# Optimization experiments

Hardware: AMD Instinct MI355X
Metric: run time of the kernel (lower is better)

The kernel has to match this reference:

```python
import jax, jax.numpy as jnp
import numpy as np


def setup_inputs() -> dict:
    key = jax.random.key(0)
    k1, k2, k3 = jax.random.split(key, 3)
    N, K = 131072, 1000
    f = jax.random.normal(k1, (N, K), dtype=jnp.float32)
    ccp = jax.random.uniform(k2, (K,), dtype=jnp.float32)
    labels = jax.random.randint(k3, (N,), 0, K, dtype=jnp.int32)
    return {"f": f, "ccp": ccp, "labels": labels, "K": K}


def reference(f, ccp, labels, K):
    # neglog[i, j] = -log_softmax(f)[i, j]
    neglog = -jax.nn.log_softmax(f, axis=1)  # [N, K]
    N = f.shape[0]
    # Per-class counts and per-class column sums (segmented reduction by label).
    counts = jax.ops.segment_sum(jnp.ones((N,), dtype=f.dtype), labels, num_segments=K)  # [K]
    sums = jax.ops.segment_sum(neglog, labels, num_segments=K)  # [K, K]
    # means[k] = mean over rows with label==k; classes with zero samples contribute 0
    # (the torch loop skips them entirely).
    safe_counts = jnp.maximum(counts, 1.0)
    means = jnp.where(counts[:, None] > 0, sums / safe_counts[:, None], 0.0)  # [K, K]
    # loss_vector = sum_k ccp[k] * means[k] ; temp[k] = -(K-1)*ccp[k]*means[k,k]
    loss_vector = ccp @ means - (K - 1) * ccp * jnp.diagonal(means)  # [K]
    # beta = +inf => max(loss_vector, -inf) == loss_vector
    final_loss = jnp.sum(loss_vector)
    weighted = counts * loss_vector  # count * loss_vector as in torch code
    return final_loss, weighted
```

## Files before the change

### kernel.cpp

```cpp
#include <hip/hip_runtime.h>
#include <math.h>


typedef float f4 __attribute__((ext_vector_type(4)));

__device__ inline float wave_reduce_sum(float v) {
    #pragma unroll
    for (int off = 32; off > 0; off >>= 1)
        v += __shfl_xor(v, off, 64);
    return v;
}

__global__ __launch_bounds__(256) void count_kernel(const int* __restrict__ labels,
                                                    float* __restrict__ counts,
                                                    int N, int K) {
    __shared__ int h[1024];
    for (int j = threadIdx.x; j < 1024; j += blockDim.x) h[j] = 0;
    __syncthreads();
    for (int i = blockIdx.x * blockDim.x + threadIdx.x; i < N;
         i += gridDim.x * blockDim.x) {
        atomicAdd(&h[labels[i]], 1);
    }
    __syncthreads();
    for (int j = threadIdx.x; j < K; j += blockDim.x) {
        int c = h[j];
        if (c) atomicAdd(&counts[j], (float)c);
    }
}

__global__ __launch_bounds__(256) void wprep_kernel(const int* __restrict__ labels,
                                                    const float* __restrict__ ccp,
                                                    const float* __restrict__ counts,
                                                    float* __restrict__ w_row, int N) {
    int i = blockIdx.x * blockDim.x + threadIdx.x;
    if (i < N) {
        int l = labels[i];
        w_row[i] = ccp[l] / counts[l];
    }
}

template <int V4>
__global__ __launch_bounds__(256) void main_kernel(
    const float* __restrict__ f, const int* __restrict__ labels,
    const float* __restrict__ w_row,
    float* __restrict__ g_multi, float* __restrict__ d_multi,
    float* __restrict__ S_acc, int N, int K) {
    __shared__ float g_sh[1024];
    __shared__ float d_sh[1024];
    __shared__ float s_sh[4];

    const int tid = threadIdx.x;
    const int lane = tid & 63;
    const int wid = tid >> 6;
    const int gwid = blockIdx.x * 4 + wid;
    const int nwaves = gridDim.x * 4;
    const int K4 = K >> 2;

    for (int j = tid; j < 1024; j += 256) { g_sh[j] = 0.f; d_sh[j] = 0.f; }
    __syncthreads();

    f4 gacc[V4];
    #pragma unroll
    for (int t = 0; t < V4; ++t) gacc[t] = (f4)(0.f);
    float s_reg = 0.f;

    f4 valsA[V4], valsB[V4];
    float wA = 0.f, wB = 0.f;
    int lA = 0, lB = 0;

    auto issue = [&](f4 (&vals)[V4], float& w, int& l, int r) {
        const f4* row4 = reinterpret_cast<const f4*>(f + (size_t)r * (size_t)K);
        #pragma unroll
        for (int t = 0; t < V4; ++t) {
            int j4 = lane + 64 * t;
            vals[t] = (j4 < K4) ? __builtin_nontemporal_load(&row4[j4]) : (f4)(0.f);
        }
        w = w_row[r];
        l = labels[r];
    };

    auto process = [&](f4 (&vals)[V4], float w, int l) {
        float e = 0.f;
        #pragma unroll
        for (int t = 0; t < V4; ++t) {
            int j4 = lane + 64 * t;
            if (j4 < K4) {
                e += __expf(vals[t].x) + __expf(vals[t].y) +
                     __expf(vals[t].z) + __expf(vals[t].w);
                gacc[t].x = fmaf(w, vals[t].x, gacc[t].x);
                gacc[t].y = fmaf(w, vals[t].y, gacc[t].y);
                gacc[t].z = fmaf(w, vals[t].z, gacc[t].z);
                gacc[t].w = fmaf(w, vals[t].w, gacc[t].w);
            }
        }
        e = wave_reduce_sum(e);
        float lse = __logf(e);
        const int j4l = l >> 2;
        const int ll = j4l & 63;
        const int tl = j4l >> 6;
        const int cl = l & 3;
        #pragma unroll
        for (int t = 0; t < V4; ++t) {
            if (lane == ll && t == tl) {
                float vl = (cl == 0) ? vals[t].x
                         : (cl == 1) ? vals[t].y
                         : (cl == 2) ? vals[t].z : vals[t].w;
                atomicAdd(&d_sh[l], lse - vl);
            }
        }
        if (lane == 0) s_reg = fmaf(w, lse, s_reg);
    };

    int ra = gwid;
    if (ra < N) {
        issue(valsA, wA, lA, ra);
        while (true) {
            int rb = ra + nwaves;
            if (rb < N) issue(valsB, wB, lB, rb);
            process(valsA, wA, lA);
            if (rb >= N) break;
            int rc = rb + nwaves;
            if (rc < N) issue(valsA, wA, lA, rc);
            process(valsB, wB, lB);
            if (rc >= N) break;
            ra = rc;
        }
    }

    if (lane == 0) s_sh[wid] = s_reg;
    #pragma unroll
    for (int t = 0; t < V4; ++t) {
        int j4 = lane + 64 * t;
        if (j4 < K4) {
            atomicAdd(&g_sh[4 * j4 + 0], gacc[t].x);
            atomicAdd(&g_sh[4 * j4 + 1], gacc[t].y);
            atomicAdd(&g_sh[4 * j4 + 2], gacc[t].z);
            atomicAdd(&g_sh[4 * j4 + 3], gacc[t].w);
        }
    }
    __syncthreads();
    const int part = (blockIdx.x & 7) * 1024;
    for (int j = tid; j < K; j += 256) {
        atomicAdd(&g_multi[part + j], g_sh[j]);
        atomicAdd(&d_multi[part + j], d_sh[j]);
    }
    if (tid == 0) {
        atomicAdd(S_acc, s_sh[0] + s_sh[1] + s_sh[2] + s_sh[3]);
    }
}

__global__ __launch_bounds__(1024) void finalize_kernel(
    const float* __restrict__ ccp, const float* __restrict__ counts,
    const float* __restrict__ g_multi, const float* __restrict__ d_multi,
    const float* __restrict__ S_acc, float* __restrict__ out, int K) {
    __shared__ float red[16];
    const int j = threadIdx.x;
    const float S = S_acc[0];

    float lv = 0.f;
    if (j < K) {
        float gj = 0.f, dj = 0.f;
        #pragma unroll
        for (int c = 0; c < 8; ++c) {
            gj += g_multi[c * 1024 + j];
            dj += d_multi[c * 1024 + j];
        }
        float cnt = counts[j];
        float dm = (cnt > 0.f) ? dj / cnt : 0.f;
        float val = S - gj - (float)(K - 1) * ccp[j] * dm;
        lv = val;
        out[1 + j] = cnt * val;
    }

    float v = wave_reduce_sum(lv);
    const int lane = j & 63;
    const int wv = j >> 6;
    if (lane == 0) red[wv] = v;
    __syncthreads();
    if (j == 0) {
        float tot = 0.f;
        for (int w2 = 0; w2 < 16; ++w2) tot += red[w2];
        out[0] = tot;
    }
}

extern "C" void kernel_launch(void* const* d_in, const int* in_sizes, int n_in,
                              void* d_out, int out_size, void* d_ws, size_t ws_size,
                              hipStream_t stream) {
    const float* f = (const float*)d_in[0];
    const float* ccp = (const float*)d_in[1];
    const int* labels = (const int*)d_in[2];
    const int K = in_sizes[1];
    const int N = in_sizes[2];

    float* ws = (float*)d_ws;
    float* counts = ws;
    float* g_multi = ws + 1024;
    float* d_multi = ws + 1024 + 8192;
    float* S_acc = ws + 1024 + 16384;
    float* w_row = ws + 32768;
    float* out = (float*)d_out;

    (void)hipMemsetAsync(d_ws, 0, (size_t)32768 * sizeof(float), stream);

    count_kernel<<<256, 256, 0, stream>>>(labels, counts, N, K);
    wprep_kernel<<<(N + 255) / 256, 256, 0, stream>>>(labels, ccp, counts, w_row, N);
    main_kernel<4><<<1024, 256, 0, stream>>>(f, labels, w_row, g_multi, d_multi,
                                             S_acc, N, K);
    finalize_kernel<<<1, 1024, 0, stream>>>(ccp, counts, g_multi, d_multi, S_acc,
                                            out, K);
}
```

Baseline: 117.8 us.

## Fuse weight prep into main kernel, triple-buffer rows, use contiguous row chunks

Removes the separate wprep kernel and its workspace buffer, computing ccp[l]/counts[l] inside the main kernel's issue step. The main loop moves from a strided row assignment to contiguous per-wave chunks and from double to triple buffering, keeping more loads in flight. It also adds a min-blocks hint to launch bounds and shrinks the memset. The aim is to save one launch plus its memory traffic and to hide more load latency, at the cost of higher register pressure and a dependent gather (labels then ccp/counts) on each row.

```diff
diff --git a/kernel.cpp b/kernel.cpp
--- a/kernel.cpp
+++ b/kernel.cpp
@@ -28,21 +28,10 @@
     }
 }
 
-__global__ __launch_bounds__(256) void wprep_kernel(const int* __restrict__ labels,
-                                                    const float* __restrict__ ccp,
-                                                    const float* __restrict__ counts,
-                                                    float* __restrict__ w_row, int N) {
-    int i = blockIdx.x * blockDim.x + threadIdx.x;
-    if (i < N) {
-        int l = labels[i];
-        w_row[i] = ccp[l] / counts[l];
-    }
-}
-
 template <int V4>
-__global__ __launch_bounds__(256) void main_kernel(
+__global__ __launch_bounds__(256, 4) void main_kernel(
     const float* __restrict__ f, const int* __restrict__ labels,
-    const float* __restrict__ w_row,
+    const float* __restrict__ ccp, const float* __restrict__ counts,
     float* __restrict__ g_multi, float* __restrict__ d_multi,
     float* __restrict__ S_acc, int N, int K) {
     __shared__ float g_sh[1024];
@@ -64,9 +53,9 @@
     for (int t = 0; t < V4; ++t) gacc[t] = (f4)(0.f);
     float s_reg = 0.f;
 
-    f4 valsA[V4], valsB[V4];
-    float wA = 0.f, wB = 0.f;
-    int lA = 0, lB = 0;
+    f4 valsA[V4], valsB[V4], valsC[V4];
+    float wA = 0.f, wB = 0.f, wC = 0.f;
+    int lA = 0, lB = 0, lC = 0;
 
     auto issue = [&](f4 (&vals)[V4], float& w, int& l, int r) {
         const f4* row4 = reinterpret_cast<const f4*>(f + (size_t)r * (size_t)K);
@@ -75,8 +64,8 @@
             int j4 = lane + 64 * t;
             vals[t] = (j4 < K4) ? __builtin_nontemporal_load(&row4[j4]) : (f4)(0.f);
         }
-        w = w_row[r];
         l = labels[r];
+        w = ccp[l] / counts[l];
     };
 
     auto process = [&](f4 (&vals)[V4], float w, int l) {
@@ -111,19 +100,24 @@
         if (lane == 0) s_reg = fmaf(w, lse, s_reg);
     };
 
-    int ra = gwid;
-    if (ra < N) {
-        issue(valsA, wA, lA, ra);
+    const int chunk = (N + nwaves - 1) / nwaves;
+    const int r0 = gwid * chunk;
+    const int n = min(chunk, N - r0);
+
+    if (n > 0) {
+        issue(valsA, wA, lA, r0);
+        if (n > 1) issue(valsB, wB, lB, r0 + 1);
+        int i = 0;
         while (true) {
-            int rb = ra + nwaves;
-            if (rb < N) issue(valsB, wB, lB, rb);
+            if (i + 2 < n) issue(valsC, wC, lC, r0 + i + 2);
             process(valsA, wA, lA);
-            if (rb >= N) break;
-            int rc = rb + nwaves;
-            if (rc < N) issue(valsA, wA, lA, rc);
+            if (++i >= n) break;
+            if (i + 2 < n) issue(valsA, wA, lA, r0 + i + 2);
             process(valsB, wB, lB);
-            if (rc >= N) break;
-            ra = rc;
+            if (++i >= n) break;
+            if (i + 2 < n) issue(valsB, wB, lB, r0 + i + 2);
+            process(valsC, wC, lC);
+            if (++i >= n) break;
         }
     }
 
@@ -198,15 +192,13 @@
     float* g_multi = ws + 1024;
     float* d_multi = ws + 1024 + 8192;
     float* S_acc = ws + 1024 + 16384;
-    float* w_row = ws + 32768;
     float* out = (float*)d_out;
 
-    (void)hipMemsetAsync(d_ws, 0, (size_t)32768 * sizeof(float), stream);
+    (void)hipMemsetAsync(d_ws, 0, (size_t)(1024 + 16384 + 1) * sizeof(float), stream);
 
     count_kernel<<<256, 256, 0, stream>>>(labels, counts, N, K);
-    wprep_kernel<<<(N + 255) / 256, 256, 0, stream>>>(labels, ccp, counts, w_row, N);
-    main_kernel<4><<<1024, 256, 0, stream>>>(f, labels, w_row, g_multi, d_multi,
-                                             S_acc, N, K);
+    main_kernel<4><<<1024, 256, 0, stream>>>(f, labels, ccp, counts, g_multi,
+                                             d_multi, S_acc, N, K);
     finalize_kernel<<<1, 1024, 0, stream>>>(ccp, counts, g_multi, d_multi, S_acc,
                                             out, K);
 }
```

Result: slower. 128.1 us (+8.7%).
